# Kernel tuning notes

Hardware: AMD Instinct MI355X
Metric: run time of the kernel (lower is better)

The kernel has to match this reference:

```python
import jax, jax.numpy as jnp
import numpy as np

N, T, n, C, C2 = 4, 8, 16384, 64, 64

def setup_inputs() -> dict:
    key = jax.random.key(0)
    k1, k2, k3, k4, k5 = jax.random.split(key, 5)
    return {
        "key_mem": jax.random.normal(k1, (N, T, n, C), dtype=jnp.float32),
        "val_mem": jax.random.normal(k2, (N, T, n, C2), dtype=jnp.float32),
        "key_cur": jax.random.normal(k3, (N, n, C), dtype=jnp.float32),
        "val_cur": jax.random.normal(k4, (N, n, C2), dtype=jnp.float32),
        "alpha": jax.random.normal(k5, (1,), dtype=jnp.float32),
    }

def reference(key_mem, val_mem, key_cur, val_cur, alpha):
    # kv_mul: contract memory tokens (T*n) -> (N, C, C2), tiny matrix
    kv_mul = jnp.einsum('btnc,btnd->bcd', key_mem, val_mem)
    # softmax over the C axis (dim=1 in torch layout (N, C, C2))
    kv_mul = jax.nn.softmax(kv_mul, axis=1)
    # out: (N, n, C) @ (N, C, C2) -> (N, n, C2)
    out = jnp.einsum('bnc,bcd->bnd', key_cur, kv_mul)
    return alpha * out + val_cur
```

## Files before the change

kernel.cpp:

```cpp
#include <hip/hip_runtime.h>
#include <math.h>

#define T_DIM   8
#define N_TOK   16384
#define C_DIM   64
#define K_TOT   (T_DIM * N_TOK)
#define N_BATCH 4

__global__ __launch_bounds__(512, 4) void k1_accum(
    const float* __restrict__ key, const float* __restrict__ val,
    float* __restrict__ part, int bpb) {
  int blk  = blockIdx.x;
  int b    = blk / bpb;
  int p    = blk % bpb;
  int wave = threadIdx.x >> 6;
  int lane = threadIdx.x & 63;
  int i = lane >> 3;
  int j = lane & 7;

  int wpb   = bpb * 8;
  int q     = p * 8 + wave;
  int steps = K_TOT / wpb;

  float acc[8][8];
#pragma unroll
  for (int a = 0; a < 8; a++)
#pragma unroll
    for (int c = 0; c < 8; c++) acc[a][c] = 0.f;

  const float4* k4 = (const float4*)key;
  const float4* v4 = (const float4*)val;
  size_t base = (size_t)b * K_TOT;

  size_t row = (base + (size_t)q) * 16;
  float4 ka = k4[row + 2 * i];
  float4 kb = k4[row + 2 * i + 1];
  float4 va = v4[row + 2 * j];
  float4 vb = v4[row + 2 * j + 1];

  int k = q + wpb;
#pragma unroll 2
  for (int s = 0; s < steps - 1; s++, k += wpb) {
    size_t r2 = (base + (size_t)k) * 16;
    float4 nka = k4[r2 + 2 * i];
    float4 nkb = k4[r2 + 2 * i + 1];
    float4 nva = v4[r2 + 2 * j];
    float4 nvb = v4[r2 + 2 * j + 1];
    {
      float kr[8] = {ka.x, ka.y, ka.z, ka.w, kb.x, kb.y, kb.z, kb.w};
      float vr[8] = {va.x, va.y, va.z, va.w, vb.x, vb.y, vb.z, vb.w};
#pragma unroll
      for (int a = 0; a < 8; a++)
#pragma unroll
        for (int c = 0; c < 8; c++)
          acc[a][c] = fmaf(kr[a], vr[c], acc[a][c]);
    }
    ka = nka; kb = nkb; va = nva; vb = nvb;
  }
  {
    float kr[8] = {ka.x, ka.y, ka.z, ka.w, kb.x, kb.y, kb.z, kb.w};
    float vr[8] = {va.x, va.y, va.z, va.w, vb.x, vb.y, vb.z, vb.w};
#pragma unroll
    for (int a = 0; a < 8; a++)
#pragma unroll
      for (int c = 0; c < 8; c++)
        acc[a][c] = fmaf(kr[a], vr[c], acc[a][c]);
  }

  __shared__ float red[2][4096];
  if (wave < 2) {
#pragma unroll
    for (int a = 0; a < 8; a++) {
      int c = 8 * i + a;
      *(float4*)&red[wave][c * 64 + 8 * j] =
          make_float4(acc[a][0], acc[a][1], acc[a][2], acc[a][3]);
      *(float4*)&red[wave][c * 64 + 8 * j + 4] =
          make_float4(acc[a][4], acc[a][5], acc[a][6], acc[a][7]);
    }
  }
  __syncthreads();
#pragma unroll
  for (int g = 1; g < 4; g++) {
    if (wave >= 2 * g && wave < 2 * g + 2) {
      int wb = wave - 2 * g;
#pragma unroll
      for (int a = 0; a < 8; a++) {
        int c = 8 * i + a;
        float4* d0 = (float4*)&red[wb][c * 64 + 8 * j];
        float4* d1 = (float4*)&red[wb][c * 64 + 8 * j + 4];
        float4 x0 = *d0, x1 = *d1;
        *d0 = make_float4(x0.x + acc[a][0], x0.y + acc[a][1],
                          x0.z + acc[a][2], x0.w + acc[a][3]);
        *d1 = make_float4(x1.x + acc[a][4], x1.y + acc[a][5],
                          x1.z + acc[a][6], x1.w + acc[a][7]);
      }
    }
    __syncthreads();
  }

  float* dst = part + (size_t)blk * 4096;
  int t = threadIdx.x;
#pragma unroll
  for (int x = 0; x < 8; x++) {
    int e = t + 512 * x;
    dst[e] = red[0][e] + red[1][e];
  }
}

__global__ __launch_bounds__(256, 4) void k2_reduce(
    const float* __restrict__ part, float* __restrict__ kv, int bpb) {
  int b  = blockIdx.x >> 6;
  int c  = blockIdx.x & 63;
  int p4 = threadIdx.x >> 6;
  int d  = threadIdx.x & 63;

  float s = 0.f;
  int iters = bpb >> 2;
  const float* src = part + (size_t)(b * bpb) * 4096 + c * 64 + d;
#pragma unroll 4
  for (int x = 0; x < iters; x++) s += src[(size_t)(p4 + 4 * x) * 4096];

  __shared__ float l[256];
  l[threadIdx.x] = s;
  __syncthreads();
  if (p4 == 0)
    kv[((size_t)b * 64 + c) * 64 + d] = l[d] + l[64 + d] + l[128 + d] + l[192 + d];
}

__global__ __launch_bounds__(64, 1) void k2b_softmax(
    const float* __restrict__ kv, float* __restrict__ P) {
  int b = blockIdx.x;
  int d = threadIdx.x;
  const float* s = kv + (size_t)b * 4096 + d;
  float v[64];
#pragma unroll
  for (int c = 0; c < 64; c++) v[c] = s[c * 64];
  float mx = v[0];
#pragma unroll
  for (int c = 1; c < 64; c++) mx = fmaxf(mx, v[c]);
  float sum = 0.f;
#pragma unroll
  for (int c = 0; c < 64; c++) {
    v[c] = __expf(v[c] - mx);
    sum += v[c];
  }
  float inv = 1.f / sum;
  float* o = P + (size_t)b * 4096 + d;
#pragma unroll
  for (int c = 0; c < 64; c++) o[c * 64] = v[c] * inv;
}

__global__ __launch_bounds__(256, 4) void k3_out(
    const float* __restrict__ P, const float* __restrict__ keyc,
    const float* __restrict__ valc, const float* __restrict__ alphap,
    float* __restrict__ out) {
  __shared__ float Ps[4096];
  __shared__ float kT[64 * 68];

  int bb = blockIdx.x >> 8;
  int mb = blockIdx.x & 255;
  int m0 = mb * 64;
  int t = threadIdx.x;

  const float4* p4 = (const float4*)(P + (size_t)bb * 4096);
  float4* ps4 = (float4*)Ps;
#pragma unroll
  for (int u = 0; u < 4; u++) ps4[t + 256 * u] = p4[t + 256 * u];

  int r  = t >> 2;
  int cb = (t & 3) * 16;
  const float* krow = keyc + ((size_t)bb * N_TOK + m0 + r) * 64;
#pragma unroll
  for (int u = 0; u < 4; u++) {
    float4 kk = *(const float4*)&krow[cb + 4 * u];
    int c = cb + 4 * u;
    kT[(c + 0) * 68 + r] = kk.x;
    kT[(c + 1) * 68 + r] = kk.y;
    kT[(c + 2) * 68 + r] = kk.z;
    kT[(c + 3) * 68 + r] = kk.w;
  }
  __syncthreads();

  int wave = t >> 6, lane = t & 63;
  int mi = lane >> 3, j = lane & 7;
  int m = wave * 16 + mi * 2;

  float acc[2][8];
#pragma unroll
  for (int a = 0; a < 2; a++)
#pragma unroll
    for (int d = 0; d < 8; d++) acc[a][d] = 0.f;

#pragma unroll 4
  for (int c = 0; c < 64; c++) {
    float2 kk = *(const float2*)&kT[c * 68 + m];
    float4 p0 = *(const float4*)&Ps[c * 64 + 8 * j];
    float4 p1 = *(const float4*)&Ps[c * 64 + 8 * j + 4];
    float pr[8] = {p0.x, p0.y, p0.z, p0.w, p1.x, p1.y, p1.z, p1.w};
#pragma unroll
    for (int d = 0; d < 8; d++) {
      acc[0][d] = fmaf(kk.x, pr[d], acc[0][d]);
      acc[1][d] = fmaf(kk.y, pr[d], acc[1][d]);
    }
  }

  float alpha = alphap[0];
#pragma unroll
  for (int a = 0; a < 2; a++) {
    size_t off = ((size_t)bb * N_TOK + m0 + m + a) * 64 + 8 * j;
    float4 v0 = *(const float4*)&valc[off];
    float4 v1 = *(const float4*)&valc[off + 4];
    float4 o0 = make_float4(fmaf(alpha, acc[a][0], v0.x),
                            fmaf(alpha, acc[a][1], v0.y),
                            fmaf(alpha, acc[a][2], v0.z),
                            fmaf(alpha, acc[a][3], v0.w));
    float4 o1 = make_float4(fmaf(alpha, acc[a][4], v1.x),
                            fmaf(alpha, acc[a][5], v1.y),
                            fmaf(alpha, acc[a][6], v1.z),
                            fmaf(alpha, acc[a][7], v1.w));
    *(float4*)&out[off] = o0;
    *(float4*)&out[off + 4] = o1;
  }
}

extern "C" void kernel_launch(void* const* d_in, const int* in_sizes, int n_in,
                              void* d_out, int out_size, void* d_ws,
                              size_t ws_size, hipStream_t stream) {
  const float* key_mem = (const float*)d_in[0];
  const float* val_mem = (const float*)d_in[1];
  const float* key_cur = (const float*)d_in[2];
  const float* val_cur = (const float*)d_in[3];
  const float* alpha   = (const float*)d_in[4];
  float* out = (float*)d_out;
  float* ws  = (float*)d_ws;

  int bpb = 128;
  while (bpb > 8 &&
         ((size_t)(N_BATCH * bpb) * 4096 + 4096 * N_BATCH) * sizeof(float) >
             ws_size)
    bpb >>= 1;

  float* part = ws;
  float* kv   = ws + (size_t)(N_BATCH * bpb) * 4096;
  float* P    = ws;

  k1_accum<<<N_BATCH * bpb, 512, 0, stream>>>(key_mem, val_mem, part, bpb);
  k2_reduce<<<256, 256, 0, stream>>>(part, kv, bpb);
  k2b_softmax<<<N_BATCH, 64, 0, stream>>>(kv, P);
  k3_out<<<N_BATCH * (N_TOK / 64), 256, 0, stream>>>(P, key_cur, val_cur,
                                                     alpha, out);
}
```

Measured before the change: 345.6 us.

## Stage key/value tiles into LDS with async global_load_lds double buffering

The accumulation kernel now gives each block a contiguous range of rows and streams 64-row key/value tiles straight into shared memory with the global_load_lds builtin, double-buffered across iterations. Threads then read their 8x8 outer-product operands from LDS instead of issuing per-wave strided global float4 loads. The intent is more coalesced, asynchronous bulk loads that overlap with the FMA work of this memory-bound reduction. In exchange it adds a block-wide barrier every tile, raises LDS use to 64KB per block, which may lower occupancy, and hardcodes the block count with no fallback when the workspace is small.

```diff
diff --git a/kernel.cpp b/kernel.cpp
--- a/kernel.cpp
+++ b/kernel.cpp
@@ -1,26 +1,36 @@
 #include <hip/hip_runtime.h>
 #include <math.h>
 
-#define T_DIM   8
 #define N_TOK   16384
-#define C_DIM   64
-#define K_TOT   (T_DIM * N_TOK)
+#define K_TOT   (8 * N_TOK)
 #define N_BATCH 4
+#define BPB     128
+#define RPB     (K_TOT / BPB)
+#define BK      64
+#define NBUF    (RPB / BK)
+
+typedef const __attribute__((address_space(1))) unsigned int* as1_u32p;
+typedef __attribute__((address_space(3))) unsigned int* as3_u32p;
+
+__device__ __forceinline__ void gload16(const float* g, float* l) {
+  __builtin_amdgcn_global_load_lds((as1_u32p)g, (as3_u32p)l, 16, 0, 0);
+}
 
 __global__ __launch_bounds__(512, 4) void k1_accum(
     const float* __restrict__ key, const float* __restrict__ val,
-    float* __restrict__ part, int bpb) {
+    float* __restrict__ part) {
+  __shared__ float lds[16384];
   int blk  = blockIdx.x;
-  int b    = blk / bpb;
-  int p    = blk % bpb;
+  int b    = blk / BPB;
+  int p    = blk % BPB;
   int wave = threadIdx.x >> 6;
   int lane = threadIdx.x & 63;
   int i = lane >> 3;
   int j = lane & 7;
 
-  int wpb   = bpb * 8;
-  int q     = p * 8 + wave;
-  int steps = K_TOT / wpb;
+  size_t row0 = (size_t)b * K_TOT + (size_t)p * RPB;
+  const float* kb = key + row0 * 64;
+  const float* vb = val + row0 * 64;
 
   float acc[8][8];
 #pragma unroll
@@ -28,46 +38,40 @@
 #pragma unroll
     for (int c = 0; c < 8; c++) acc[a][c] = 0.f;
 
-  const float4* k4 = (const float4*)key;
-  const float4* v4 = (const float4*)val;
-  size_t base = (size_t)b * K_TOT;
-
-  size_t row = (base + (size_t)q) * 16;
-  float4 ka = k4[row + 2 * i];
-  float4 kb = k4[row + 2 * i + 1];
-  float4 va = v4[row + 2 * j];
-  float4 vb = v4[row + 2 * j + 1];
-
-  int k = q + wpb;
-#pragma unroll 2
-  for (int s = 0; s < steps - 1; s++, k += wpb) {
-    size_t r2 = (base + (size_t)k) * 16;
-    float4 nka = k4[r2 + 2 * i];
-    float4 nkb = k4[r2 + 2 * i + 1];
-    float4 nva = v4[r2 + 2 * j];
-    float4 nvb = v4[r2 + 2 * j + 1];
-    {
-      float kr[8] = {ka.x, ka.y, ka.z, ka.w, kb.x, kb.y, kb.z, kb.w};
-      float vr[8] = {va.x, va.y, va.z, va.w, vb.x, vb.y, vb.z, vb.w};
+  auto stage = [&](int t, int buf) {
+    const float* kg = kb + (size_t)t * (BK * 64);
+    const float* vg = vb + (size_t)t * (BK * 64);
+    float* dl = &lds[buf * 8192];
+    gload16(kg + wave * 256 + lane * 4,        dl + wave * 256);
+    gload16(kg + (wave + 8) * 256 + lane * 4,  dl + (wave + 8) * 256);
+    gload16(vg + wave * 256 + lane * 4,        dl + 4096 + wave * 256);
+    gload16(vg + (wave + 8) * 256 + lane * 4,  dl + 4096 + (wave + 8) * 256);
+  };
+
+  stage(0, 0);
+  for (int t = 0; t < NBUF; t++) {
+    __syncthreads();
+    if (t + 1 < NBUF) stage(t + 1, (t + 1) & 1);
+    const float* ks = &lds[(t & 1) * 8192];
+    const float* vs = ks + 4096;
+#pragma unroll
+    for (int rr = 0; rr < BK / 8; rr++) {
+      int r = wave + rr * 8;
+      float4 k0 = *(const float4*)&ks[r * 64 + 8 * i];
+      float4 k1 = *(const float4*)&ks[r * 64 + 8 * i + 4];
+      float4 v0 = *(const float4*)&vs[r * 64 + 8 * j];
+      float4 v1 = *(const float4*)&vs[r * 64 + 8 * j + 4];
+      float kr[8] = {k0.x, k0.y, k0.z, k0.w, k1.x, k1.y, k1.z, k1.w};
+      float vr[8] = {v0.x, v0.y, v0.z, v0.w, v1.x, v1.y, v1.z, v1.w};
 #pragma unroll
       for (int a = 0; a < 8; a++)
 #pragma unroll
         for (int c = 0; c < 8; c++)
           acc[a][c] = fmaf(kr[a], vr[c], acc[a][c]);
     }
-    ka = nka; kb = nkb; va = nva; vb = nvb;
-  }
-  {
-    float kr[8] = {ka.x, ka.y, ka.z, ka.w, kb.x, kb.y, kb.z, kb.w};
-    float vr[8] = {va.x, va.y, va.z, va.w, vb.x, vb.y, vb.z, vb.w};
-#pragma unroll
-    for (int a = 0; a < 8; a++)
-#pragma unroll
-      for (int c = 0; c < 8; c++)
-        acc[a][c] = fmaf(kr[a], vr[c], acc[a][c]);
-  }
-
-  __shared__ float red[2][4096];
+  }
+
+  float (*red)[4096] = (float(*)[4096])lds;
   if (wave < 2) {
 #pragma unroll
     for (int a = 0; a < 8; a++) {
@@ -234,18 +238,12 @@
   float* out = (float*)d_out;
   float* ws  = (float*)d_ws;
 
-  int bpb = 128;
-  while (bpb > 8 &&
-         ((size_t)(N_BATCH * bpb) * 4096 + 4096 * N_BATCH) * sizeof(float) >
-             ws_size)
-    bpb >>= 1;
-
   float* part = ws;
-  float* kv   = ws + (size_t)(N_BATCH * bpb) * 4096;
+  float* kv   = ws + (size_t)(N_BATCH * BPB) * 4096;
   float* P    = ws;
 
-  k1_accum<<<N_BATCH * bpb, 512, 0, stream>>>(key_mem, val_mem, part, bpb);
-  k2_reduce<<<256, 256, 0, stream>>>(part, kv, bpb);
+  k1_accum<<<N_BATCH * BPB, 512, 0, stream>>>(key_mem, val_mem, part);
+  k2_reduce<<<256, 256, 0, stream>>>(part, kv, BPB);
   k2b_softmax<<<N_BATCH, 64, 0, stream>>>(kv, P);
   k3_out<<<N_BATCH * (N_TOK / 64), 256, 0, stream>>>(P, key_cur, val_cur,
                                                      alpha, out);
```

After: 343.1 us. No clear change (-0.7%).
